# Kernel optimization log

Hardware: AMD Instinct MI355X
Metric: run time of the kernel (lower is better)

## Reference

```python
import jax, jax.numpy as jnp
import numpy as np

D_MODEL = 1024
NUM_HEADS = 16
THETA = 10000.0
BATCH = 2
SEQ = 2048


def _rope(x, pos, theta):
    # x: (b, h, l, d), pos: (l,)
    d = x.shape[-1]
    half = d // 2
    inv_freq = theta ** (-(jnp.arange(half, dtype=x.dtype) / half))  # theta^(-2k/d)
    ang = pos.astype(x.dtype)[:, None] * inv_freq[None, :]  # (l, half)
    cos, sin = jnp.cos(ang), jnp.sin(ang)
    x1, x2 = x[..., ::2], x[..., 1::2]
    r1 = x1 * cos - x2 * sin
    r2 = x1 * sin + x2 * cos
    return jnp.stack([r1, r2], axis=-1).reshape(x.shape)


def setup_inputs() -> dict:
    key = jax.random.key(0)
    k1, k2, k3 = jax.random.split(key, 3)
    x = jax.random.normal(k1, (BATCH, SEQ, D_MODEL), dtype=jnp.float32)
    W_kqv = jax.random.normal(k2, (3 * D_MODEL, D_MODEL), dtype=jnp.float32) * (1.0 / np.sqrt(D_MODEL))
    W_o = jax.random.normal(k3, (D_MODEL, D_MODEL), dtype=jnp.float32) * (1.0 / np.sqrt(D_MODEL))
    return {"x": x, "W_kqv": W_kqv, "W_o": W_o}


def reference(x, W_kqv, W_o):
    b, L, _ = x.shape
    h = NUM_HEADS
    d = D_MODEL // h
    kqv = x @ W_kqv.T  # (b, l, 3*d_model)
    K, Q, V = jnp.split(kqv, 3, axis=-1)  # chunk order in source: K, Q, V
    # (b, l, h*d) -> (b, h, l, d)
    Q = Q.reshape(b, L, h, d).transpose(0, 2, 1, 3)
    K = K.reshape(b, L, h, d).transpose(0, 2, 1, 3)
    V = V.reshape(b, L, h, d).transpose(0, 2, 1, 3)
    pos = jnp.arange(L)
    Q = _rope(Q, pos, THETA)
    K = _rope(K, pos, THETA)
    scores = jnp.einsum('bhqd,bhkd->bhqk', Q, K) / jnp.sqrt(jnp.asarray(d, x.dtype))
    causal = jnp.tril(jnp.ones((L, L), dtype=bool))
    scores = jnp.where(causal, scores, jnp.finfo(scores.dtype).min)
    probs = jax.nn.softmax(scores, axis=-1)
    out = jnp.einsum('bhqk,bhkd->bhqd', probs, V)
    out = out.transpose(0, 2, 1, 3).reshape(b, L, h * d)
    return out @ W_o.T
```

## Files before the change

kernel.cpp:

```cpp
#include <hip/hip_runtime.h>
#include <hip/hip_bf16.h>
#include <stdint.h>

#define BATCH 2
#define SEQ 2048
#define DMODEL 1024
#define NHEADS 16
#define HDIM 64
#define MROWS (BATCH*SEQ)
#define N3 (3*DMODEL)

typedef __attribute__((ext_vector_type(8))) __bf16 bf16x8;
typedef __attribute__((ext_vector_type(4))) float f32x4;

__device__ __forceinline__ ushort f2b(float f) {
  uint32_t u = __builtin_bit_cast(uint32_t, f);
  uint32_t r = (u + 0x7FFFu + ((u >> 16) & 1u)) >> 16;
  return (ushort)r;
}
__device__ __forceinline__ float b2f(ushort h) {
  return __builtin_bit_cast(float, (uint32_t)h << 16);
}
__device__ __forceinline__ float exp2_hw(float x) {
  float r;
  asm("v_exp_f32 %0, %1" : "=v"(r) : "v"(x));
  return r;
}
__device__ __forceinline__ uint32_t cvtpk(float a, float b) {
  uint32_t r;
  asm("v_cvt_pk_bf16_f32 %0, %1, %2" : "=v"(r) : "v"(a), "v"(b));
  return r;
}

__global__ void f2b3_kernel(const float* __restrict__ a, const float* __restrict__ b,
                            const float* __restrict__ c,
                            ushort* __restrict__ oa, ushort* __restrict__ ob,
                            ushort* __restrict__ oc, int na, int nb, int nc) {
  int i = blockIdx.x * blockDim.x + threadIdx.x;
  const float* src; ushort* dst; int off;
  if (i < na)           { src = a; dst = oa; off = i; }
  else if (i < na + nb) { src = b; dst = ob; off = i - na; }
  else if (i < na + nb + nc) { src = c; dst = oc; off = i - na - nb; }
  else return;
  float4 v = ((const float4*)src)[off];
  uint32_t lo = cvtpk(v.x, v.y), hi_ = cvtpk(v.z, v.w);
  ((uint2*)dst)[off] = make_uint2(lo, hi_);
}

template<int OUTF>
__global__ __launch_bounds__(256)
void gemm_bt(const ushort* __restrict__ A, const ushort* __restrict__ Bw,
             void* __restrict__ Cv, int M, int N, int K) {
  __shared__ __align__(16) ushort As[128*32];
  __shared__ __align__(16) ushort Bs[128*32];
  const int tid  = threadIdx.x;
  const int wid  = tid >> 6;
  const int lane = tid & 63;
  const int wr   = wid >> 1, wc = wid & 1;
  const int l16  = lane & 15, lhi = lane >> 4;
  const int nb   = N >> 7;
  const int brow = (blockIdx.x / nb) << 7;
  const int bcol = (blockIdx.x % nb) << 7;

  f32x4 acc[4][4] = {};

  for (int k0 = 0; k0 < K; k0 += 32) {
    __syncthreads();
#pragma unroll
    for (int it = 0; it < 2; ++it) {
      const int cb    = (wid * 2 + it) * 64;
      const int chunk = cb + lane;
      const int r     = chunk >> 2;
      const int c8    = chunk & 3;
      const ushort* ga = A  + (size_t)(brow + r) * K + k0 + c8 * 8;
      const ushort* gb = Bw + (size_t)(bcol + r) * K + k0 + c8 * 8;
      __builtin_amdgcn_global_load_lds(
          (const __attribute__((address_space(1))) void*)ga,
          (__attribute__((address_space(3))) void*)(As + cb * 8), 16, 0, 0);
      __builtin_amdgcn_global_load_lds(
          (const __attribute__((address_space(1))) void*)gb,
          (__attribute__((address_space(3))) void*)(Bs + cb * 8), 16, 0, 0);
    }
    __syncthreads();

    bf16x8 af[4], bfr[4];
#pragma unroll
    for (int m = 0; m < 4; ++m)
      af[m] = *(const bf16x8*)(As + (wr*64 + m*16 + l16)*32 + lhi*8);
#pragma unroll
    for (int n = 0; n < 4; ++n)
      bfr[n] = *(const bf16x8*)(Bs + (wc*64 + n*16 + l16)*32 + lhi*8);
#pragma unroll
    for (int m = 0; m < 4; ++m)
#pragma unroll
      for (int n = 0; n < 4; ++n)
        acc[m][n] = __builtin_amdgcn_mfma_f32_16x16x32_bf16(af[m], bfr[n], acc[m][n], 0, 0, 0);
  }

#pragma unroll
  for (int m = 0; m < 4; ++m)
#pragma unroll
    for (int n = 0; n < 4; ++n)
#pragma unroll
      for (int r = 0; r < 4; ++r) {
        const int row = brow + wr*64 + m*16 + lhi*4 + r;
        const int col = bcol + wc*64 + n*16 + l16;
        if (OUTF) ((float*)Cv)[(size_t)row * N + col] = acc[m][n][r];
        else      ((ushort*)Cv)[(size_t)row * N + col] = f2b(acc[m][n][r]);
      }
}

__global__ __launch_bounds__(256)
void prep_kernel(const ushort* __restrict__ kqv,
                 ushort* __restrict__ qb, ushort* __restrict__ kb, ushort* __restrict__ vt) {
  __shared__ ushort tile[64][65];
  if (blockIdx.x < 1024) {
    int bid = blockIdx.x;
    int lt = bid & 31, bh = bid >> 5;
    int b = bh >> 4, h = bh & 15;
    int tid = threadIdx.x;
    int r = tid >> 2, cq = tid & 3;
    size_t gbase = ((size_t)(b * SEQ + lt * 64 + r)) * N3 + 2 * DMODEL + h * HDIM + cq * 16;
#pragma unroll
    for (int j = 0; j < 16; ++j) tile[r][cq * 16 + j] = kqv[gbase + j];
    __syncthreads();
    int d = tid >> 2;
    size_t obase = ((size_t)(bh * HDIM + d)) * SEQ + lt * 64 + cq * 16;
#pragma unroll
    for (int j = 0; j < 16; ++j) vt[obase + j] = tile[cq * 16 + j][d];
  } else {
    const float SC = 0.18033688011112042f;
    int idx = (blockIdx.x - 1024) * 256 + threadIdx.x;
    int i  = idx & 31;
    int h  = (idx >> 5) & 15;
    int bl = idx >> 9;
    int l  = bl & (SEQ - 1);
    int b  = bl >> 11;
    float inv = exp2f((float)i * -0.4152410118609203f);
    float ang = (float)l * inv;
    float s, c;
    sincosf(ang, &s, &c);
    size_t base = (size_t)bl * N3 + h * HDIM + 2 * i;
    uint32_t kp = *(const uint32_t*)(kqv + base);
    uint32_t qp = *(const uint32_t*)(kqv + base + DMODEL);
    float k1 = b2f((ushort)(kp & 0xffff)), k2 = b2f((ushort)(kp >> 16));
    float q1 = b2f((ushort)(qp & 0xffff)), q2 = b2f((ushort)(qp >> 16));
    float kr1 = k1 * c - k2 * s, kr2 = k1 * s + k2 * c;
    float qr1 = (q1 * c - q2 * s) * SC, qr2 = (q1 * s + q2 * c) * SC;
    size_t ob = ((size_t)(b * NHEADS + h) * SEQ + l) * HDIM + 2 * i;
    *(uint32_t*)(kb + ob) = cvtpk(kr1, kr2);
    *(uint32_t*)(qb + ob) = cvtpk(qr1, qr2);
  }
}

__global__ __launch_bounds__(256, 2)
void attn_kernel(const ushort* __restrict__ qb, const ushort* __restrict__ kb,
                 const ushort* __restrict__ vt, ushort* __restrict__ ao) {
  __shared__ __align__(16) ushort Kbuf[3][4096];
  __shared__ __align__(16) ushort Vbuf[3][4096];
  __shared__ __align__(16) ushort plds[4][1024];
  const int bid = blockIdx.x;
  const int bh = bid & 31;
  const int p  = bid >> 5;
  const int qtA = p, qtB = 31 - p;

  const int wid = threadIdx.x >> 6, lane = threadIdx.x & 63;
  const int l16 = lane & 15, lhi = lane >> 4;
  const int r0A = qtA * 64 + wid * 16;
  const int r0B = qtB * 64 + wid * 16;

  const ushort* Q  = qb + (size_t)bh * SEQ * HDIM;
  const ushort* Kp = kb + (size_t)bh * SEQ * HDIM;
  const ushort* Vp = vt + (size_t)bh * HDIM * SEQ;

  bf16x8 qfA[2], qfB[2];
#pragma unroll
  for (int kc = 0; kc < 2; ++kc) {
    qfA[kc] = *(const bf16x8*)(Q + (size_t)(r0A + l16) * HDIM + kc * 32 + lhi * 8);
    qfB[kc] = *(const bf16x8*)(Q + (size_t)(r0B + l16) * HDIM + kc * 32 + lhi * 8);
  }

  float mqA = -3.0e38f, lsA = 0.0f, mqB = -3.0e38f, lsB = 0.0f;
  f32x4 oA[4] = {}, oB[4] = {};

  char* pbase = (char*)&plds[wid][0];
  const int swz = (l16 & 7) << 4;

  auto STAGE = [&](int buf, int kt) {
    ushort* kd = &Kbuf[buf][0];
    ushort* vd = &Vbuf[buf][0];
    const ushort* kg = Kp + (size_t)kt * 64 * HDIM;
    const ushort* vg = Vp + kt * 64;
#pragma unroll
    for (int it = 0; it < 2; ++it) {
      const int cb = it * 256 + wid * 64;
      const int ci = cb + lane;
      const int row = ci >> 3;
      const int sl  = (ci & 7) ^ (row & 7);
      __builtin_amdgcn_global_load_lds(
          (const __attribute__((address_space(1))) void*)(kg + row * HDIM + sl * 8),
          (__attribute__((address_space(3))) void*)(kd + cb * 8), 16, 0, 0);
      __builtin_amdgcn_global_load_lds(
          (const __attribute__((address_space(1))) void*)(vg + (size_t)row * SEQ + sl * 8),
          (__attribute__((address_space(3))) void*)(vd + cb * 8), 16, 0, 0);
    }
  };

  auto BODY = [&](const char* kc_, const char* vc_, bf16x8 (&qf)[2],
                  float& mq, float& lsq, f32x4 (&o)[4], int r0, int qt, int kt) {
    f32x4 s[4];
#pragma unroll
    for (int n = 0; n < 4; ++n) {
      const int kvr = n * 16 + l16;
      bf16x8 kf0 = *(const bf16x8*)(kc_ + kvr*128 + ((lhi     ^ (kvr&7)) * 16));
      bf16x8 kf1 = *(const bf16x8*)(kc_ + kvr*128 + (((4+lhi) ^ (kvr&7)) * 16));
      f32x4 z = 0.0f;
      z = __builtin_amdgcn_mfma_f32_16x16x32_bf16(kf0, qf[0], z, 0, 0, 0);
      z = __builtin_amdgcn_mfma_f32_16x16x32_bf16(kf1, qf[1], z, 0, 0, 0);
      s[n] = z;
    }
    if (kt == qt) {
#pragma unroll
      for (int n = 0; n < 4; ++n)
#pragma unroll
        for (int r = 0; r < 4; ++r)
          if (kt*64 + n*16 + lhi*4 + r > r0 + l16) s[n][r] = -3.0e38f;
    }
    float t0 = fmaxf(fmaxf(s[0][0], s[0][1]), fmaxf(s[0][2], s[0][3]));
    float t1 = fmaxf(fmaxf(s[1][0], s[1][1]), fmaxf(s[1][2], s[1][3]));
    float t2 = fmaxf(fmaxf(s[2][0], s[2][1]), fmaxf(s[2][2], s[2][3]));
    float t3 = fmaxf(fmaxf(s[3][0], s[3][1]), fmaxf(s[3][2], s[3][3]));
    float pmx = fmaxf(fmaxf(t0, t1), fmaxf(t2, t3));
    pmx = fmaxf(pmx, __shfl_xor(pmx, 16));
    pmx = fmaxf(pmx, __shfl_xor(pmx, 32));

    if (!__all(pmx <= mq)) {
      float mn = fmaxf(mq, pmx);
      float alpha = exp2_hw(mq - mn);
      mq = mn;
      lsq *= alpha;
      float alphaT[4];
#pragma unroll
      for (int r = 0; r < 4; ++r)
        alphaT[r] = __shfl(alpha, lhi * 4 + r);
#pragma unroll
      for (int f = 0; f < 4; ++f)
#pragma unroll
        for (int r = 0; r < 4; ++r)
          o[f][r] *= alphaT[r];
    }

    float ps = 0.0f;
#pragma unroll
    for (int n = 0; n < 4; ++n)
#pragma unroll
      for (int r = 0; r < 4; ++r) {
        float pv = exp2_hw(s[n][r] - mq);
        s[n][r] = pv;
        ps += pv;
      }
    ps += __shfl_xor(ps, 16);
    ps += __shfl_xor(ps, 32);
    lsq += ps;

#pragma unroll
    for (int n = 0; n < 4; ++n) {
      uint32_t w0 = cvtpk(s[n][0], s[n][1]);
      uint32_t w1 = cvtpk(s[n][2], s[n][3]);
      int kvloc = n*16 + lhi*4;
      *(uint32_t*)(pbase + ((l16*128 + kvloc*2) ^ swz))       = w0;
      *(uint32_t*)(pbase + ((l16*128 + (kvloc+2)*2) ^ swz))   = w1;
    }
    bf16x8 pa0 = *(const bf16x8*)(pbase + ((l16*128 + 0*64 + lhi*16) ^ swz));
    bf16x8 pa1 = *(const bf16x8*)(pbase + ((l16*128 + 1*64 + lhi*16) ^ swz));

#pragma unroll
    for (int f = 0; f < 4; ++f) {
      const int dr = f * 16 + l16;
      bf16x8 vf0 = *(const bf16x8*)(vc_ + dr*128 + ((lhi     ^ (dr&7)) * 16));
      bf16x8 vf1 = *(const bf16x8*)(vc_ + dr*128 + (((4+lhi) ^ (dr&7)) * 16));
      o[f] = __builtin_amdgcn_mfma_f32_16x16x32_bf16(pa0, vf0, o[f], 0, 0, 0);
      o[f] = __builtin_amdgcn_mfma_f32_16x16x32_bf16(pa1, vf1, o[f], 0, 0, 0);
    }
  };

  STAGE(0, 0);
  STAGE(1, 1);

  for (int kt = 0; kt <= qtB; ++kt) {
    if (kt < qtB) asm volatile("s_waitcnt vmcnt(4)" ::: "memory");
    else          asm volatile("s_waitcnt vmcnt(0)" ::: "memory");
    __builtin_amdgcn_s_barrier();
    __builtin_amdgcn_sched_barrier(0);

    if (kt + 2 <= qtB) STAGE((kt + 2) % 3, kt + 2);

    const char* kc_ = (const char*)&Kbuf[kt % 3][0];
    const char* vc_ = (const char*)&Vbuf[kt % 3][0];
    BODY(kc_, vc_, qfB, mqB, lsB, oB, r0B, qtB, kt);
    if (kt <= qtA)
      BODY(kc_, vc_, qfA, mqA, lsA, oA, r0A, qtA, kt);

    __builtin_amdgcn_sched_barrier(0);
  }

  const int b = bh >> 4, h = bh & 15;
  float invA = 1.0f / lsA, invB = 1.0f / lsB;
#pragma unroll
  for (int r = 0; r < 4; ++r) {
    float wA = __shfl(invA, lhi * 4 + r);
    float wB = __shfl(invB, lhi * 4 + r);
    size_t baseA = ((size_t)(b * SEQ + r0A + lhi*4 + r)) * DMODEL + h * HDIM + l16;
    size_t baseB = ((size_t)(b * SEQ + r0B + lhi*4 + r)) * DMODEL + h * HDIM + l16;
#pragma unroll
    for (int f = 0; f < 4; ++f) {
      ao[baseA + f*16] = f2b(oA[f][r] * wA);
      ao[baseB + f*16] = f2b(oB[f][r] * wB);
    }
  }
}

extern "C" void kernel_launch(void* const* d_in, const int* in_sizes, int n_in,
                              void* d_out, int out_size, void* d_ws, size_t ws_size,
                              hipStream_t stream) {
  const float* x    = (const float*)d_in[0];
  const float* wkqv = (const float*)d_in[1];
  const float* wo   = (const float*)d_in[2];
  float* out = (float*)d_out;

  ushort* xb   = (ushort*)d_ws;
  ushort* wkb  = xb  + (size_t)MROWS * DMODEL;
  ushort* wob  = wkb + (size_t)N3 * DMODEL;
  ushort* kqv  = wob + (size_t)DMODEL * DMODEL;
  ushort* qb   = kqv + (size_t)MROWS * N3;
  ushort* kb   = qb  + (size_t)MROWS * DMODEL;
  ushort* vt   = kb  + (size_t)MROWS * DMODEL;
  ushort* attn = xb;

  int nx = MROWS * DMODEL / 4, nw = N3 * DMODEL / 4, no = DMODEL * DMODEL / 4;
  f2b3_kernel<<<(nx + nw + no) / 256, 256, 0, stream>>>(x, wkqv, wo, xb, wkb, wob, nx, nw, no);

  gemm_bt<0><<<(MROWS/128) * (N3/128), 256, 0, stream>>>(xb, wkb, (void*)kqv, MROWS, N3, DMODEL);

  prep_kernel<<<1024 + (MROWS * NHEADS * 32) / 256, 256, 0, stream>>>(kqv, qb, kb, vt);

  attn_kernel<<<512, 256, 0, stream>>>(qb, kb, vt, attn);

  gemm_bt<1><<<(MROWS/128) * (DMODEL/128), 256, 0, stream>>>(attn, wob, (void*)out, MROWS, DMODEL, DMODEL);
}
```

Measured before the change: 126.7 us.

## Fuse RoPE and Q/K head-layout write into the QKV GEMM epilogue

Adds a specialized QKV GEMM whose epilogue applies rotary embedding and the softmax scale to the Q and K tiles. It writes them directly in per-head layout, with the rotation partner fetched by a lane shuffle. V is written to a compact buffer, and a separate small kernel transposes it. This removes the full kqv intermediate round-trip and the RoPE part of the prep kernel, at the cost of per-element sincos inside the GEMM epilogue and scattered 2-byte stores.

```diff
diff --git a/kernel.cpp b/kernel.cpp
--- a/kernel.cpp
+++ b/kernel.cpp
@@ -45,6 +45,113 @@
   float4 v = ((const float4*)src)[off];
   uint32_t lo = cvtpk(v.x, v.y), hi_ = cvtpk(v.z, v.w);
   ((uint2*)dst)[off] = make_uint2(lo, hi_);
+}
+
+__global__ __launch_bounds__(256)
+void gemm_kqv(const ushort* __restrict__ A, const ushort* __restrict__ Bw,
+              ushort* __restrict__ kb, ushort* __restrict__ qb, ushort* __restrict__ vtmp) {
+  const int M = MROWS, N = N3, K = DMODEL;
+  __shared__ __align__(16) ushort As[128*32];
+  __shared__ __align__(16) ushort Bs[128*32];
+  const int tid  = threadIdx.x;
+  const int wid  = tid >> 6;
+  const int lane = tid & 63;
+  const int wr   = wid >> 1, wc = wid & 1;
+  const int l16  = lane & 15, lhi = lane >> 4;
+  const int nb   = N >> 7;
+  const int brow = (blockIdx.x / nb) << 7;
+  const int bcol = (blockIdx.x % nb) << 7;
+
+  f32x4 acc[4][4] = {};
+
+  for (int k0 = 0; k0 < K; k0 += 32) {
+    __syncthreads();
+#pragma unroll
+    for (int it = 0; it < 2; ++it) {
+      const int cb    = (wid * 2 + it) * 64;
+      const int chunk = cb + lane;
+      const int r     = chunk >> 2;
+      const int c8    = chunk & 3;
+      const ushort* ga = A  + (size_t)(brow + r) * K + k0 + c8 * 8;
+      const ushort* gb = Bw + (size_t)(bcol + r) * K + k0 + c8 * 8;
+      __builtin_amdgcn_global_load_lds(
+          (const __attribute__((address_space(1))) void*)ga,
+          (__attribute__((address_space(3))) void*)(As + cb * 8), 16, 0, 0);
+      __builtin_amdgcn_global_load_lds(
+          (const __attribute__((address_space(1))) void*)gb,
+          (__attribute__((address_space(3))) void*)(Bs + cb * 8), 16, 0, 0);
+    }
+    __syncthreads();
+
+    bf16x8 af[4], bfr[4];
+#pragma unroll
+    for (int m = 0; m < 4; ++m)
+      af[m] = *(const bf16x8*)(As + (wr*64 + m*16 + l16)*32 + lhi*8);
+#pragma unroll
+    for (int n = 0; n < 4; ++n)
+      bfr[n] = *(const bf16x8*)(Bs + (wc*64 + n*16 + l16)*32 + lhi*8);
+#pragma unroll
+    for (int m = 0; m < 4; ++m)
+#pragma unroll
+      for (int n = 0; n < 4; ++n)
+        acc[m][n] = __builtin_amdgcn_mfma_f32_16x16x32_bf16(af[m], bfr[n], acc[m][n], 0, 0, 0);
+  }
+
+  const int matsel = bcol >> 10;
+  if (matsel == 2) {
+    const int dmbase = (bcol - 2048) + wc * 64;
+#pragma unroll
+    for (int m = 0; m < 4; ++m)
+#pragma unroll
+      for (int n = 0; n < 4; ++n)
+#pragma unroll
+        for (int r = 0; r < 4; ++r) {
+          const int row = brow + wr*64 + m*16 + lhi*4 + r;
+          vtmp[(size_t)row * DMODEL + dmbase + n*16 + l16] = f2b(acc[m][n][r]);
+        }
+  } else {
+    const float SC = (matsel == 1) ? 0.18033688011112042f : 1.0f;
+    ushort* dst = (matsel == 1) ? qb : kb;
+    const int h = ((bcol & 1023) >> 6) + wc;
+    const int bq = brow >> 11;
+    const float ssign = (l16 & 1) ? 1.0f : -1.0f;
+#pragma unroll
+    for (int n = 0; n < 4; ++n) {
+      const int d = n*16 + l16;
+      const float inv = exp2f((float)(d >> 1) * -0.4152410118609203f);
+#pragma unroll
+      for (int m = 0; m < 4; ++m)
+#pragma unroll
+        for (int r = 0; r < 4; ++r) {
+          const int row = brow + wr*64 + m*16 + lhi*4 + r;
+          const int l = row & (SEQ - 1);
+          float sn, cs;
+          __sincosf((float)l * inv, &sn, &cs);
+          float val  = acc[m][n][r];
+          float part = __shfl_xor(val, 1);
+          float out  = (val * cs + part * sn * ssign) * SC;
+          dst[((size_t)((bq * NHEADS + h) * SEQ + l)) * HDIM + d] = f2b(out);
+        }
+    }
+  }
+}
+
+__global__ __launch_bounds__(256)
+void vtrans_kernel(const ushort* __restrict__ vtmp, ushort* __restrict__ vt) {
+  __shared__ ushort tile[64][65];
+  int bid = blockIdx.x;
+  int lt = bid & 31, bh = bid >> 5;
+  int b = bh >> 4, h = bh & 15;
+  int tid = threadIdx.x;
+  int r = tid >> 2, cq = tid & 3;
+  size_t gbase = ((size_t)(b * SEQ + lt * 64 + r)) * DMODEL + h * HDIM + cq * 16;
+#pragma unroll
+  for (int j = 0; j < 16; ++j) tile[r][cq * 16 + j] = vtmp[gbase + j];
+  __syncthreads();
+  int d = tid >> 2;
+  size_t obase = ((size_t)(bh * HDIM + d)) * SEQ + lt * 64 + cq * 16;
+#pragma unroll
+  for (int j = 0; j < 16; ++j) vt[obase + j] = tile[cq * 16 + j][d];
 }
 
 template<int OUTF>
@@ -110,49 +217,6 @@
       }
 }
 
-__global__ __launch_bounds__(256)
-void prep_kernel(const ushort* __restrict__ kqv,
-                 ushort* __restrict__ qb, ushort* __restrict__ kb, ushort* __restrict__ vt) {
-  __shared__ ushort tile[64][65];
-  if (blockIdx.x < 1024) {
-    int bid = blockIdx.x;
-    int lt = bid & 31, bh = bid >> 5;
-    int b = bh >> 4, h = bh & 15;
-    int tid = threadIdx.x;
-    int r = tid >> 2, cq = tid & 3;
-    size_t gbase = ((size_t)(b * SEQ + lt * 64 + r)) * N3 + 2 * DMODEL + h * HDIM + cq * 16;
-#pragma unroll
-    for (int j = 0; j < 16; ++j) tile[r][cq * 16 + j] = kqv[gbase + j];
-    __syncthreads();
-    int d = tid >> 2;
-    size_t obase = ((size_t)(bh * HDIM + d)) * SEQ + lt * 64 + cq * 16;
-#pragma unroll
-    for (int j = 0; j < 16; ++j) vt[obase + j] = tile[cq * 16 + j][d];
-  } else {
-    const float SC = 0.18033688011112042f;
-    int idx = (blockIdx.x - 1024) * 256 + threadIdx.x;
-    int i  = idx & 31;
-    int h  = (idx >> 5) & 15;
-    int bl = idx >> 9;
-    int l  = bl & (SEQ - 1);
-    int b  = bl >> 11;
-    float inv = exp2f((float)i * -0.4152410118609203f);
-    float ang = (float)l * inv;
-    float s, c;
-    sincosf(ang, &s, &c);
-    size_t base = (size_t)bl * N3 + h * HDIM + 2 * i;
-    uint32_t kp = *(const uint32_t*)(kqv + base);
-    uint32_t qp = *(const uint32_t*)(kqv + base + DMODEL);
-    float k1 = b2f((ushort)(kp & 0xffff)), k2 = b2f((ushort)(kp >> 16));
-    float q1 = b2f((ushort)(qp & 0xffff)), q2 = b2f((ushort)(qp >> 16));
-    float kr1 = k1 * c - k2 * s, kr2 = k1 * s + k2 * c;
-    float qr1 = (q1 * c - q2 * s) * SC, qr2 = (q1 * s + q2 * c) * SC;
-    size_t ob = ((size_t)(b * NHEADS + h) * SEQ + l) * HDIM + 2 * i;
-    *(uint32_t*)(kb + ob) = cvtpk(kr1, kr2);
-    *(uint32_t*)(qb + ob) = cvtpk(qr1, qr2);
-  }
-}
-
 __global__ __launch_bounds__(256, 2)
 void attn_kernel(const ushort* __restrict__ qb, const ushort* __restrict__ kb,
                  const ushort* __restrict__ vt, ushort* __restrict__ ao) {
@@ -331,8 +395,8 @@
   ushort* xb   = (ushort*)d_ws;
   ushort* wkb  = xb  + (size_t)MROWS * DMODEL;
   ushort* wob  = wkb + (size_t)N3 * DMODEL;
-  ushort* kqv  = wob + (size_t)DMODEL * DMODEL;
-  ushort* qb   = kqv + (size_t)MROWS * N3;
+  ushort* vtmp = wob + (size_t)DMODEL * DMODEL;
+  ushort* qb   = vtmp + (size_t)MROWS * DMODEL;
   ushort* kb   = qb  + (size_t)MROWS * DMODEL;
   ushort* vt   = kb  + (size_t)MROWS * DMODEL;
   ushort* attn = xb;
@@ -340,9 +404,9 @@
   int nx = MROWS * DMODEL / 4, nw = N3 * DMODEL / 4, no = DMODEL * DMODEL / 4;
   f2b3_kernel<<<(nx + nw + no) / 256, 256, 0, stream>>>(x, wkqv, wo, xb, wkb, wob, nx, nw, no);
 
-  gemm_bt<0><<<(MROWS/128) * (N3/128), 256, 0, stream>>>(xb, wkb, (void*)kqv, MROWS, N3, DMODEL);
-
-  prep_kernel<<<1024 + (MROWS * NHEADS * 32) / 256, 256, 0, stream>>>(kqv, qb, kb, vt);
+  gemm_kqv<<<(MROWS/128) * (N3/128), 256, 0, stream>>>(xb, wkb, kb, qb, vtmp);
+
+  vtrans_kernel<<<BATCH * NHEADS * (SEQ / 64), 256, 0, stream>>>(vtmp, vt);
 
   attn_kernel<<<512, 256, 0, stream>>>(qb, kb, vt, attn);
 
```

New measurement: 134.1 us. 5.9% more time.
